# Optimization experiments

Measured on AMD Instinct MI355X. Metric: run time of the kernel, lower is better.

The kernel has to match this reference:

```python
import jax, jax.numpy as jnp
import numpy as np

N_NODES = 50000
N_EDGES = 600000


def gcn_conv(x, src, dst, W, b, num_nodes):
    # x: [N, Cin] -> [N, Cout]; symmetric-normalized GCN with self-loops
    h = x @ W  # [N, Cout]
    loop = jnp.arange(num_nodes, dtype=src.dtype)
    s = jnp.concatenate([src, loop])
    d = jnp.concatenate([dst, loop])
    ones = jnp.ones(s.shape[0], dtype=h.dtype)
    deg = jax.ops.segment_sum(ones, d, num_segments=num_nodes)  # in-degree incl self-loop
    dinv = jnp.where(deg > 0, jax.lax.rsqrt(deg), 0.0)
    norm = dinv[s] * dinv[d]  # [E+N]
    msg = h[s] * norm[:, None]  # gather + scale
    out = jax.ops.segment_sum(msg, d, num_segments=num_nodes)  # scatter-add
    return out + b


def setup_inputs() -> dict:
    key = jax.random.key(0)
    k1, k2, k3, k4 = jax.random.split(key, 4)
    x = jax.random.normal(k1, (N_NODES, 128), dtype=jnp.float32)
    edge_index = jax.random.randint(k2, (2, N_EDGES), 0, N_NODES, dtype=jnp.int64)
    W1 = jax.random.normal(k3, (128, 128), dtype=jnp.float32) * (1.0 / np.sqrt(128))
    b1 = jnp.zeros((128,), dtype=jnp.float32)
    W2 = jax.random.normal(k4, (128, 64), dtype=jnp.float32) * (1.0 / np.sqrt(128))
    b2 = jnp.zeros((64,), dtype=jnp.float32)
    return {"x": x, "edge_index": edge_index, "W1": W1, "b1": b1, "W2": W2, "b2": b2}


def reference(x, edge_index, W1, b1, W2, b2):
    src, dst = edge_index[0], edge_index[1]
    h = gcn_conv(x, src, dst, W1, b1, N_NODES)
    h = jax.nn.relu(h)
    out = gcn_conv(h, src, dst, W2, b2, N_NODES)
    return out
```

## Files before the change

### kernel.cpp

```cpp
#include <hip/hip_runtime.h>
#include <hip/hip_fp16.h>
#include <cstddef>
#include <cstdint>

#define N_NODES 50000
#define N_EDGES 600000
#define M_TILES 3125
#define GEMM_BLKS 782
#define NBUCK 196
#define BUCK_CAP 4096
#define ROUTE_EDGES 2048
#define ROUTE_BLKS 293

typedef short bf16x8 __attribute__((ext_vector_type(8)));
typedef float f32x4 __attribute__((ext_vector_type(4)));


__device__ __forceinline__ unsigned short f32_to_bf16(float x) {
  unsigned u = __float_as_uint(x);
  u += 0x7FFFu + ((u >> 16) & 1u);
  return (unsigned short)(u >> 16);
}
__device__ __forceinline__ float bf16_to_f32(unsigned short h) {
  return __uint_as_float((unsigned)h << 16);
}
__device__ __forceinline__ float bf16_lo(unsigned g) {
  return __uint_as_float(g << 16);
}
__device__ __forceinline__ float bf16_hi(unsigned g) {
  return __uint_as_float(g & 0xFFFF0000u);
}
__device__ __forceinline__ float pk_w(unsigned pk) {
  return __half2float(__ushort_as_half((unsigned short)(pk >> 16)));
}

__device__ __forceinline__ void split8(const float* __restrict__ p, bf16x8& hi,
                                       bf16x8& lo) {
  const float4 v0 = *(const float4*)p;
  const float4 v1 = *(const float4*)(p + 4);
  float v[8] = {v0.x, v0.y, v0.z, v0.w, v1.x, v1.y, v1.z, v1.w};
#pragma unroll
  for (int i = 0; i < 8; i++) {
    const unsigned short h = f32_to_bf16(v[i]);
    hi[i] = (short)h;
    lo[i] = (short)f32_to_bf16(v[i] - bf16_to_f32(h));
  }
}

template <int COUT>
__device__ __forceinline__ void gemm_body(const int wtile, const int lane,
                                          const float* __restrict__ X,
                                          const unsigned short* __restrict__ Wph,
                                          const unsigned short* __restrict__ Wpl,
                                          unsigned short* __restrict__ Hs) {
  constexpr int CT = COUT / 16;
  const int m = lane & 15;
  const int q = lane >> 4;

  f32x4 acc[CT];
#pragma unroll
  for (int ct = 0; ct < CT; ct++) acc[ct] = {0.f, 0.f, 0.f, 0.f};

  const float* xp = X + (size_t)(wtile * 16 + m) * 128 + q * 8;

#pragma unroll
  for (int ks = 0; ks < 4; ks++) {
    bf16x8 ah, al;
    split8(xp + ks * 32, ah, al);
#pragma unroll
    for (int ct = 0; ct < CT; ct++) {
      const size_t bo = ((size_t)(ct * 4 + ks) * 64 + lane) * 8;
      const bf16x8 bh = *(const bf16x8*)(Wph + bo);
      const bf16x8 bl = *(const bf16x8*)(Wpl + bo);
      acc[ct] = __builtin_amdgcn_mfma_f32_16x16x32_bf16(ah, bh, acc[ct], 0, 0, 0);
      acc[ct] = __builtin_amdgcn_mfma_f32_16x16x32_bf16(al, bh, acc[ct], 0, 0, 0);
      acc[ct] = __builtin_amdgcn_mfma_f32_16x16x32_bf16(ah, bl, acc[ct], 0, 0, 0);
    }
  }
#pragma unroll
  for (int ct = 0; ct < CT; ct++) {
#pragma unroll
    for (int r = 0; r < 4; r++) {
      const int orow = wtile * 16 + q * 4 + r;
      Hs[(size_t)orow * COUT + ct * 16 + m] = f32_to_bf16(acc[ct][r]);
    }
  }
}

__device__ __forceinline__ void wpack_body(const int i,
                                           const float* __restrict__ W1,
                                           const float* __restrict__ W2,
                                           unsigned short* __restrict__ w1h,
                                           unsigned short* __restrict__ w1l,
                                           unsigned short* __restrict__ w2h,
                                           unsigned short* __restrict__ w2l) {
  const float* W;
  unsigned short *wh, *wl;
  int o, cout;
  if (i < 16384) {
    W = W1; wh = w1h; wl = w1l; o = i; cout = 128;
  } else {
    W = W2; wh = w2h; wl = w2l; o = i - 16384; cout = 64;
  }
  const int j = o & 7;
  const int ln = (o >> 3) & 63;
  const int t = o >> 9;
  const int ks = t & 3;
  const int ct = t >> 2;
  const int k = ks * 32 + (ln >> 4) * 8 + j;
  const int n = ct * 16 + (ln & 15);
  const float v = W[k * cout + n];
  const unsigned short h = f32_to_bf16(v);
  wh[o] = h;
  wl[o] = f32_to_bf16(v - bf16_to_f32(h));
}

__global__ __launch_bounds__(256) void k_prep_route(
    const float* __restrict__ W1, const float* __restrict__ W2,
    unsigned short* __restrict__ w1h, unsigned short* __restrict__ w1l,
    unsigned short* __restrict__ w2h, unsigned short* __restrict__ w2l,
    const int* __restrict__ src, const int* __restrict__ dst,
    int* __restrict__ cursor, int* __restrict__ counts,
    unsigned* __restrict__ routed) {
  __shared__ int hist[NBUCK];
  __shared__ int lcur[NBUCK];
  const int tid = threadIdx.x;
  if (blockIdx.x < 96) {
    wpack_body(blockIdx.x * 256 + tid, W1, W2, w1h, w1l, w2h, w2l);
  } else {
    const int rb = blockIdx.x - 96;
    for (int t = tid; t < NBUCK; t += 256) hist[t] = 0;
    __syncthreads();
    unsigned packed[8];
    bool cvalid[2];
    const int base = rb * ROUTE_EDGES;
#pragma unroll
    for (int c = 0; c < 2; c++) {
      const int i4 = base + c * 1024 + tid * 4;
      cvalid[c] = (i4 < N_EDGES);
      if (cvalid[c]) {
        const int4 d4 = *(const int4*)(dst + i4);
        const int4 s4 = *(const int4*)(src + i4);
        packed[c * 4 + 0] = ((unsigned)d4.x << 16) | (unsigned)s4.x;
        packed[c * 4 + 1] = ((unsigned)d4.y << 16) | (unsigned)s4.y;
        packed[c * 4 + 2] = ((unsigned)d4.z << 16) | (unsigned)s4.z;
        packed[c * 4 + 3] = ((unsigned)d4.w << 16) | (unsigned)s4.w;
#pragma unroll
        for (int j = 0; j < 4; j++) {
          const unsigned pk = packed[c * 4 + j];
          atomicAdd(&hist[pk >> 24], 1);
          atomicAdd(&counts[pk >> 16], 1);
        }
      }
    }
    __syncthreads();
    for (int t = tid; t < NBUCK; t += 256)
      lcur[t] = t * BUCK_CAP + atomicAdd(&cursor[t], hist[t]);
    __syncthreads();
#pragma unroll
    for (int c = 0; c < 2; c++) {
      if (cvalid[c]) {
#pragma unroll
        for (int j = 0; j < 4; j++) {
          const unsigned pk = packed[c * 4 + j];
          const int slot = atomicAdd(&lcur[pk >> 24], 1);
          routed[slot] = pk;
        }
      }
    }
  }
}

__global__ __launch_bounds__(256) void k_bsort_gemm128(
    const unsigned* __restrict__ routed, const int* __restrict__ cursor,
    const int* __restrict__ counts, int* __restrict__ start,
    int* __restrict__ sorted_src, const float* __restrict__ X,
    const unsigned short* __restrict__ Wph,
    const unsigned short* __restrict__ Wpl, unsigned short* __restrict__ Hs) {
  __shared__ unsigned ebuf[BUCK_CAP];
  __shared__ int h2[256];
  __shared__ int c2[256];
  const int tid = threadIdx.x;
  if (blockIdx.x < NBUCK) {
    const int b = blockIdx.x;
    const int n = cursor[b];
    for (int i = tid; i < n; i += 256) ebuf[i] = routed[b * BUCK_CAP + i];
    h2[tid] = 0;
    __syncthreads();
    for (int i = tid; i < n; i += 256)
      atomicAdd(&h2[(ebuf[i] >> 16) & 255], 1);
    __syncthreads();
    const int own = h2[tid];
    for (int s = 1; s < 256; s <<= 1) {
      const int t = (tid >= s) ? h2[tid - s] : 0;
      __syncthreads();
      h2[tid] += t;
      __syncthreads();
    }
    const int pfx = h2[tid] - own;
    c2[tid] = pfx;
    const int d = b * 256 + tid;
    if (d < N_NODES) start[d] = b * BUCK_CAP + pfx;
    __syncthreads();
    for (int i = tid; i < n; i += 256) {
      const unsigned pk = ebuf[i];
      const int r = atomicAdd(&c2[(pk >> 16) & 255], 1);
      const unsigned si = pk & 0xFFFFu;
      const float rs = rsqrtf((float)counts[si] + 1.0f);
      const unsigned hb = (unsigned)__half_as_ushort(__float2half(rs));
      sorted_src[b * BUCK_CAP + r] = (int)(si | (hb << 16));
    }
  } else {
    const int wtile = (blockIdx.x - NBUCK) * 4 + (tid >> 6);
    if (wtile < M_TILES) gemm_body<128>(wtile, tid & 63, X, Wph, Wpl, Hs);
  }
}

__global__ __launch_bounds__(256) void k_agg128_gemm64(
    const unsigned* __restrict__ Hb, const int* __restrict__ counts,
    const int* __restrict__ start, const int* __restrict__ sorted_src,
    const float* __restrict__ bias, const unsigned short* __restrict__ Wph,
    const unsigned short* __restrict__ Wpl, unsigned short* __restrict__ Hs) {
  __shared__ float a1s[16][132];
  const int lane = threadIdx.x & 63;
  const int wave = threadIdx.x >> 6;
  const int h = lane >> 5;
  const int c = lane & 31;
  const uint2* __restrict__ Hb2 = (const uint2*)Hb;
  const float4 bb = ((const float4*)bias)[c];
  const int vbase = blockIdx.x * 16 + wave * 4;

  const int v0 = vbase + h, v1 = vbase + 2 + h;
  const int deg0 = counts[v0], deg1 = counts[v1];
  const int e00 = start[v0], e01 = start[v1];
  const float dv0 = rsqrtf((float)deg0 + 1.f);
  const float dv1 = rsqrtf((float)deg1 + 1.f);
  const uint2 gs0 = Hb2[(size_t)v0 * 32 + c];
  const uint2 gs1 = Hb2[(size_t)v1 * 32 + c];
  const int pk0 = (c < deg0) ? sorted_src[e00 + c] : 0;
  const int pk1 = (c < deg1) ? sorted_src[e01 + c] : 0;

#pragma unroll
  for (int p = 0; p < 2; p++) {
    const int deg = p ? deg1 : deg0;
    const int e0 = p ? e01 : e00;
    const float dv = p ? dv1 : dv0;
    const uint2 gs = p ? gs1 : gs0;
    const int pk = p ? pk1 : pk0;

    const int dA = __shfl(deg, 0);
    const int dB = __shfl(deg, 32);
    const int mm = max(dA, dB);
    const int m = min(mm, 32);
    const float dv2 = dv * dv;
    float a0 = bf16_lo(gs.x) * dv2;
    float a1 = bf16_hi(gs.x) * dv2;
    float a2 = bf16_lo(gs.y) * dv2;
    float a3 = bf16_hi(gs.y) * dv2;

    for (int j = 0; j < m; j += 8) {
      unsigned pkt[8];
      float w[8];
      uint2 g[8];
#pragma unroll
      for (int t = 0; t < 8; t++)
        pkt[t] = (unsigned)__shfl(pk, (lane & 32) | (j + t));
#pragma unroll
      for (int t = 0; t < 8; t++)
        g[t] = Hb2[(size_t)(pkt[t] & 0xFFFFu) * 32 + c];
#pragma unroll
      for (int t = 0; t < 8; t++) w[t] = pk_w(pkt[t]) * dv;
#pragma unroll
      for (int t = 0; t < 8; t++) {
        a0 += bf16_lo(g[t].x) * w[t];
        a1 += bf16_hi(g[t].x) * w[t];
        a2 += bf16_lo(g[t].y) * w[t];
        a3 += bf16_hi(g[t].y) * w[t];
      }
    }
    for (int base = 32; base < mm; base += 32) {
      int pk2 = 0;
      if (base + c < deg) pk2 = sorted_src[e0 + base + c];
      const int lim = min(32, mm - base);
      for (int k = 0; k < lim; k++) {
        const unsigned pt = (unsigned)__shfl(pk2, (lane & 32) | k);
        const uint2 g = Hb2[(size_t)(pt & 0xFFFFu) * 32 + c];
        const float w = pk_w(pt) * dv;
        a0 += bf16_lo(g.x) * w;
        a1 += bf16_hi(g.x) * w;
        a2 += bf16_lo(g.y) * w;
        a3 += bf16_hi(g.y) * w;
      }
    }
    float4 r;
    r.x = fmaxf(a0 + bb.x, 0.f);
    r.y = fmaxf(a1 + bb.y, 0.f);
    r.z = fmaxf(a2 + bb.z, 0.f);
    r.w = fmaxf(a3 + bb.w, 0.f);
    *(float4*)&a1s[wave * 4 + 2 * p + h][c * 4] = r;
  }
  __syncthreads();

  const int ct = wave;
  const int m2 = lane & 15;
  const int q = lane >> 4;
  f32x4 acc = {0.f, 0.f, 0.f, 0.f};
#pragma unroll
  for (int ks = 0; ks < 4; ks++) {
    bf16x8 ah, al;
    split8(&a1s[m2][ks * 32 + q * 8], ah, al);
    const size_t bo = ((size_t)(ct * 4 + ks) * 64 + lane) * 8;
    const bf16x8 bh = *(const bf16x8*)(Wph + bo);
    const bf16x8 bl = *(const bf16x8*)(Wpl + bo);
    acc = __builtin_amdgcn_mfma_f32_16x16x32_bf16(ah, bh, acc, 0, 0, 0);
    acc = __builtin_amdgcn_mfma_f32_16x16x32_bf16(al, bh, acc, 0, 0, 0);
    acc = __builtin_amdgcn_mfma_f32_16x16x32_bf16(ah, bl, acc, 0, 0, 0);
  }
#pragma unroll
  for (int r = 0; r < 4; r++) {
    const int orow = blockIdx.x * 16 + q * 4 + r;
    Hs[(size_t)orow * 64 + ct * 16 + m2] = f32_to_bf16(acc[r]);
  }
}

__global__ __launch_bounds__(256) void k_agg64(
    const unsigned* __restrict__ Hb, const int* __restrict__ counts,
    const int* __restrict__ start, const int* __restrict__ sorted_src,
    const float* __restrict__ bias, float* __restrict__ out) {
  const int lane = threadIdx.x & 63;
  const int wave = threadIdx.x >> 6;
  const int qq = lane >> 4;
  const int c = lane & 15;
  const uint2* __restrict__ Hb2 = (const uint2*)Hb;
  const float4 bb = ((const float4*)bias)[c];

  const int v = blockIdx.x * 16 + wave * 4 + qq;
  const int deg = counts[v];
  const int e0 = start[v];
  const float dv = rsqrtf((float)deg + 1.0f);
  const uint2 gs = Hb2[(size_t)v * 16 + c];
  const int pk0 = (c < deg) ? sorted_src[e0 + c] : 0;
  const int pk1 = (c + 16 < deg) ? sorted_src[e0 + c + 16] : 0;

  const int d0 = __shfl(deg, 0);
  const int d1 = __shfl(deg, 16);
  const int d2 = __shfl(deg, 32);
  const int d3 = __shfl(deg, 48);
  const int mm = max(max(d0, d1), max(d2, d3));
  const int m = min(mm, 32);
  const float dv2 = dv * dv;
  float a0 = bf16_lo(gs.x) * dv2;
  float a1 = bf16_hi(gs.x) * dv2;
  float a2 = bf16_lo(gs.y) * dv2;
  float a3 = bf16_hi(gs.y) * dv2;

#pragma unroll
  for (int jb = 0; jb < 4; jb++) {
    if (jb * 8 < m) {
      unsigned pkt[8];
      float w[8];
      uint2 g[8];
#pragma unroll
      for (int t = 0; t < 8; t++) {
        const int e = jb * 8 + t;
        const int srcl = (lane & 48) | (e & 15);
        pkt[t] = (unsigned)__shfl((jb < 2) ? pk0 : pk1, srcl);
      }
#pragma unroll
      for (int t = 0; t < 8; t++)
        g[t] = Hb2[(size_t)(pkt[t] & 0xFFFFu) * 16 + c];
#pragma unroll
      for (int t = 0; t < 8; t++) w[t] = pk_w(pkt[t]) * dv;
#pragma unroll
      for (int t = 0; t < 8; t++) {
        a0 += bf16_lo(g[t].x) * w[t];
        a1 += bf16_hi(g[t].x) * w[t];
        a2 += bf16_lo(g[t].y) * w[t];
        a3 += bf16_hi(g[t].y) * w[t];
      }
    }
  }
  for (int base = 32; base < mm; base += 16) {
    int pk2 = 0;
    if (base + c < deg) pk2 = sorted_src[e0 + base + c];
    const int lim = min(16, mm - base);
    for (int k = 0; k < lim; k++) {
      const unsigned pt = (unsigned)__shfl(pk2, (lane & 48) | k);
      const uint2 g = Hb2[(size_t)(pt & 0xFFFFu) * 16 + c];
      const float w = pk_w(pt) * dv;
      a0 += bf16_lo(g.x) * w;
      a1 += bf16_hi(g.x) * w;
      a2 += bf16_lo(g.y) * w;
      a3 += bf16_hi(g.y) * w;
    }
  }
  float4 r;
  r.x = a0 + bb.x;
  r.y = a1 + bb.y;
  r.z = a2 + bb.z;
  r.w = a3 + bb.w;
  ((float4*)out)[(size_t)v * 16 + c] = r;
}


extern "C" void kernel_launch(void* const* d_in, const int* in_sizes, int n_in,
                              void* d_out, int out_size, void* d_ws, size_t ws_size,
                              hipStream_t stream) {
  const float* x = (const float*)d_in[0];
  const int* ei = (const int*)d_in[1];
  const float* W1 = (const float*)d_in[2];
  const float* b1 = (const float*)d_in[3];
  const float* W2 = (const float*)d_in[4];
  const float* b2 = (const float*)d_in[5];
  const int* src = ei;
  const int* dst = ei + N_EDGES;

  char* p = (char*)d_ws;
  auto alloc = [&](size_t bytes) {
    char* q = p;
    p += (bytes + 255) & ~(size_t)255;
    return q;
  };
  int* cursor = (int*)alloc((size_t)NBUCK * 4);
  int* counts = (int*)alloc((size_t)N_NODES * 4);
  unsigned* routed = (unsigned*)alloc((size_t)NBUCK * BUCK_CAP * 4);
  int* sorted_src = (int*)alloc((size_t)NBUCK * BUCK_CAP * 4);
  int* start = (int*)alloc((size_t)N_NODES * 4);
  unsigned short* w1h = (unsigned short*)alloc(16384 * 2);
  unsigned short* w1l = (unsigned short*)alloc(16384 * 2);
  unsigned short* w2h = (unsigned short*)alloc(8192 * 2);
  unsigned short* w2l = (unsigned short*)alloc(8192 * 2);
  unsigned short* h1b = (unsigned short*)alloc((size_t)N_NODES * 128 * 2);
  unsigned short* h2b = (unsigned short*)alloc((size_t)N_NODES * 64 * 2);

  const size_t zlen = (size_t)((char*)counts - (char*)cursor) + (size_t)N_NODES * 4;
  hipMemsetAsync(cursor, 0, zlen, stream);
  hipLaunchKernelGGL(k_prep_route, dim3(96 + ROUTE_BLKS), dim3(256), 0, stream,
                     W1, W2, w1h, w1l, w2h, w2l, src, dst, cursor, counts,
                     routed);
  hipLaunchKernelGGL(k_bsort_gemm128, dim3(NBUCK + GEMM_BLKS), dim3(256), 0,
                     stream, routed, cursor, counts, start, sorted_src, x, w1h,
                     w1l, h1b);
  hipLaunchKernelGGL(k_agg128_gemm64, dim3(M_TILES), dim3(256), 0, stream,
                     (const unsigned*)h1b, counts, start, sorted_src, b1, w2h,
                     w2l, h2b);
  hipLaunchKernelGGL(k_agg64, dim3(M_TILES), dim3(256), 0, stream,
                     (const unsigned*)h2b, counts, start, sorted_src, b2,
                     (float*)d_out);
}
```

Before: 170.0 us.

## Derive degree counts from bucket histogram and defer source-norm packing to aggregation

```diff
diff --git a/kernel.cpp b/kernel.cpp
--- a/kernel.cpp
+++ b/kernel.cpp
@@ -32,6 +32,9 @@
 }
 __device__ __forceinline__ float pk_w(unsigned pk) {
   return __half2float(__ushort_as_half((unsigned short)(pk >> 16)));
+}
+__device__ __forceinline__ int pack_si(int si, float dinv) {
+  return si | ((int)__half_as_ushort(__float2half(dinv)) << 16);
 }
 
 __device__ __forceinline__ void split8(const float* __restrict__ p, bf16x8& hi,
@@ -120,8 +123,7 @@
     unsigned short* __restrict__ w1h, unsigned short* __restrict__ w1l,
     unsigned short* __restrict__ w2h, unsigned short* __restrict__ w2l,
     const int* __restrict__ src, const int* __restrict__ dst,
-    int* __restrict__ cursor, int* __restrict__ counts,
-    unsigned* __restrict__ routed) {
+    int* __restrict__ cursor, unsigned* __restrict__ routed) {
   __shared__ int hist[NBUCK];
   __shared__ int lcur[NBUCK];
   const int tid = threadIdx.x;
@@ -146,11 +148,8 @@
         packed[c * 4 + 2] = ((unsigned)d4.z << 16) | (unsigned)s4.z;
         packed[c * 4 + 3] = ((unsigned)d4.w << 16) | (unsigned)s4.w;
 #pragma unroll
-        for (int j = 0; j < 4; j++) {
-          const unsigned pk = packed[c * 4 + j];
-          atomicAdd(&hist[pk >> 24], 1);
-          atomicAdd(&counts[pk >> 16], 1);
-        }
+        for (int j = 0; j < 4; j++)
+          atomicAdd(&hist[packed[c * 4 + j] >> 24], 1);
       }
     }
     __syncthreads();
@@ -173,7 +172,7 @@
 
 __global__ __launch_bounds__(256) void k_bsort_gemm128(
     const unsigned* __restrict__ routed, const int* __restrict__ cursor,
-    const int* __restrict__ counts, int* __restrict__ start,
+    int* __restrict__ counts, int* __restrict__ start,
     int* __restrict__ sorted_src, const float* __restrict__ X,
     const unsigned short* __restrict__ Wph,
     const unsigned short* __restrict__ Wpl, unsigned short* __restrict__ Hs) {
@@ -200,15 +199,15 @@
     const int pfx = h2[tid] - own;
     c2[tid] = pfx;
     const int d = b * 256 + tid;
-    if (d < N_NODES) start[d] = b * BUCK_CAP + pfx;
+    if (d < N_NODES) {
+      counts[d] = own;
+      start[d] = b * BUCK_CAP + pfx;
+    }
     __syncthreads();
     for (int i = tid; i < n; i += 256) {
       const unsigned pk = ebuf[i];
       const int r = atomicAdd(&c2[(pk >> 16) & 255], 1);
-      const unsigned si = pk & 0xFFFFu;
-      const float rs = rsqrtf((float)counts[si] + 1.0f);
-      const unsigned hb = (unsigned)__half_as_ushort(__float2half(rs));
-      sorted_src[b * BUCK_CAP + r] = (int)(si | (hb << 16));
+      sorted_src[b * BUCK_CAP + r] = (int)(pk & 0xFFFFu);
     }
   } else {
     const int wtile = (blockIdx.x - NBUCK) * 4 + (tid >> 6);
@@ -218,7 +217,7 @@
 
 __global__ __launch_bounds__(256) void k_agg128_gemm64(
     const unsigned* __restrict__ Hb, const int* __restrict__ counts,
-    const int* __restrict__ start, const int* __restrict__ sorted_src,
+    const int* __restrict__ start, int* __restrict__ sorted_src,
     const float* __restrict__ bias, const unsigned short* __restrict__ Wph,
     const unsigned short* __restrict__ Wpl, unsigned short* __restrict__ Hs) {
   __shared__ float a1s[16][132];
@@ -237,8 +236,18 @@
   const float dv1 = rsqrtf((float)deg1 + 1.f);
   const uint2 gs0 = Hb2[(size_t)v0 * 32 + c];
   const uint2 gs1 = Hb2[(size_t)v1 * 32 + c];
-  const int pk0 = (c < deg0) ? sorted_src[e00 + c] : 0;
-  const int pk1 = (c < deg1) ? sorted_src[e01 + c] : 0;
+  int si0 = 0, si1 = 0;
+  float di0 = 0.f, di1 = 0.f;
+  if (c < deg0) {
+    si0 = sorted_src[e00 + c];
+    di0 = rsqrtf((float)counts[si0] + 1.f);
+  }
+  if (c < deg1) {
+    si1 = sorted_src[e01 + c];
+    di1 = rsqrtf((float)counts[si1] + 1.f);
+  }
+  if (c < deg0) sorted_src[e00 + c] = pack_si(si0, di0);
+  if (c < deg1) sorted_src[e01 + c] = pack_si(si1, di1);
 
 #pragma unroll
   for (int p = 0; p < 2; p++) {
@@ -246,7 +255,8 @@
     const int e0 = p ? e01 : e00;
     const float dv = p ? dv1 : dv0;
     const uint2 gs = p ? gs1 : gs0;
-    const int pk = p ? pk1 : pk0;
+    const int si = p ? si1 : si0;
+    const float wi = (p ? di1 : di0) * dv;
 
     const int dA = __shfl(deg, 0);
     const int dB = __shfl(deg, 32);
@@ -259,17 +269,16 @@
     float a3 = bf16_hi(gs.y) * dv2;
 
     for (int j = 0; j < m; j += 8) {
-      unsigned pkt[8];
+      int s[8];
       float w[8];
       uint2 g[8];
 #pragma unroll
-      for (int t = 0; t < 8; t++)
-        pkt[t] = (unsigned)__shfl(pk, (lane & 32) | (j + t));
-#pragma unroll
-      for (int t = 0; t < 8; t++)
-        g[t] = Hb2[(size_t)(pkt[t] & 0xFFFFu) * 32 + c];
-#pragma unroll
-      for (int t = 0; t < 8; t++) w[t] = pk_w(pkt[t]) * dv;
+      for (int t = 0; t < 8; t++) {
+        s[t] = __shfl(si, (lane & 32) | (j + t));
+        w[t] = __shfl(wi, (lane & 32) | (j + t));
+      }
+#pragma unroll
+      for (int t = 0; t < 8; t++) g[t] = Hb2[(size_t)s[t] * 32 + c];
 #pragma unroll
       for (int t = 0; t < 8; t++) {
         a0 += bf16_lo(g[t].x) * w[t];
@@ -279,13 +288,19 @@
       }
     }
     for (int base = 32; base < mm; base += 32) {
-      int pk2 = 0;
-      if (base + c < deg) pk2 = sorted_src[e0 + base + c];
+      int sit = 0;
+      float dit = 0.f;
+      if (base + c < deg) {
+        sit = sorted_src[e0 + base + c];
+        dit = rsqrtf((float)counts[sit] + 1.0f);
+        sorted_src[e0 + base + c] = pack_si(sit, dit);
+      }
+      const float wit = dit * dv;
       const int lim = min(32, mm - base);
       for (int k = 0; k < lim; k++) {
-        const unsigned pt = (unsigned)__shfl(pk2, (lane & 32) | k);
-        const uint2 g = Hb2[(size_t)(pt & 0xFFFFu) * 32 + c];
-        const float w = pk_w(pt) * dv;
+        const int s = __shfl(sit, (lane & 32) | k);
+        const float w = __shfl(wit, (lane & 32) | k);
+        const uint2 g = Hb2[(size_t)s * 32 + c];
         a0 += bf16_lo(g.x) * w;
         a1 += bf16_hi(g.x) * w;
         a2 += bf16_lo(g.y) * w;
@@ -422,9 +437,9 @@
     return q;
   };
   int* cursor = (int*)alloc((size_t)NBUCK * 4);
-  int* counts = (int*)alloc((size_t)N_NODES * 4);
   unsigned* routed = (unsigned*)alloc((size_t)NBUCK * BUCK_CAP * 4);
   int* sorted_src = (int*)alloc((size_t)NBUCK * BUCK_CAP * 4);
+  int* counts = (int*)alloc((size_t)N_NODES * 4);
   int* start = (int*)alloc((size_t)N_NODES * 4);
   unsigned short* w1h = (unsigned short*)alloc(16384 * 2);
   unsigned short* w1l = (unsigned short*)alloc(16384 * 2);
@@ -433,11 +448,9 @@
   unsigned short* h1b = (unsigned short*)alloc((size_t)N_NODES * 128 * 2);
   unsigned short* h2b = (unsigned short*)alloc((size_t)N_NODES * 64 * 2);
 
-  const size_t zlen = (size_t)((char*)counts - (char*)cursor) + (size_t)N_NODES * 4;
-  hipMemsetAsync(cursor, 0, zlen, stream);
+  hipMemsetAsync(cursor, 0, (size_t)NBUCK * 4, stream);
   hipLaunchKernelGGL(k_prep_route, dim3(96 + ROUTE_BLKS), dim3(256), 0, stream,
-                     W1, W2, w1h, w1l, w2h, w2l, src, dst, cursor, counts,
-                     routed);
+                     W1, W2, w1h, w1l, w2h, w2l, src, dst, cursor, routed);
   hipLaunchKernelGGL(k_bsort_gemm128, dim3(NBUCK + GEMM_BLKS), dim3(256), 0,
                      stream, routed, cursor, counts, start, sorted_src, x, w1h,
                      w1l, h1b);
```

Result: faster. 146.9 us (-13.6%).

## Derive degrees from bucket histogram and defer dinv packing to first aggregation

Applied to the files above, without the earlier changes.

```diff
diff --git a/kernel.cpp b/kernel.cpp
--- a/kernel.cpp
+++ b/kernel.cpp
@@ -120,8 +120,7 @@
     unsigned short* __restrict__ w1h, unsigned short* __restrict__ w1l,
     unsigned short* __restrict__ w2h, unsigned short* __restrict__ w2l,
     const int* __restrict__ src, const int* __restrict__ dst,
-    int* __restrict__ cursor, int* __restrict__ counts,
-    unsigned* __restrict__ routed) {
+    int* __restrict__ cursor, unsigned* __restrict__ routed) {
   __shared__ int hist[NBUCK];
   __shared__ int lcur[NBUCK];
   const int tid = threadIdx.x;
@@ -146,11 +145,8 @@
         packed[c * 4 + 2] = ((unsigned)d4.z << 16) | (unsigned)s4.z;
         packed[c * 4 + 3] = ((unsigned)d4.w << 16) | (unsigned)s4.w;
 #pragma unroll
-        for (int j = 0; j < 4; j++) {
-          const unsigned pk = packed[c * 4 + j];
-          atomicAdd(&hist[pk >> 24], 1);
-          atomicAdd(&counts[pk >> 16], 1);
-        }
+        for (int j = 0; j < 4; j++)
+          atomicAdd(&hist[packed[c * 4 + j] >> 24], 1);
       }
     }
     __syncthreads();
@@ -173,7 +169,7 @@
 
 __global__ __launch_bounds__(256) void k_bsort_gemm128(
     const unsigned* __restrict__ routed, const int* __restrict__ cursor,
-    const int* __restrict__ counts, int* __restrict__ start,
+    int2* __restrict__ meta, unsigned short* __restrict__ dinvh,
     int* __restrict__ sorted_src, const float* __restrict__ X,
     const unsigned short* __restrict__ Wph,
     const unsigned short* __restrict__ Wpl, unsigned short* __restrict__ Hs) {
@@ -200,15 +196,15 @@
     const int pfx = h2[tid] - own;
     c2[tid] = pfx;
     const int d = b * 256 + tid;
-    if (d < N_NODES) start[d] = b * BUCK_CAP + pfx;
+    if (d < N_NODES) {
+      meta[d] = make_int2(own, b * BUCK_CAP + pfx);
+      dinvh[d] = __half_as_ushort(__float2half(rsqrtf((float)own + 1.0f)));
+    }
     __syncthreads();
     for (int i = tid; i < n; i += 256) {
       const unsigned pk = ebuf[i];
       const int r = atomicAdd(&c2[(pk >> 16) & 255], 1);
-      const unsigned si = pk & 0xFFFFu;
-      const float rs = rsqrtf((float)counts[si] + 1.0f);
-      const unsigned hb = (unsigned)__half_as_ushort(__float2half(rs));
-      sorted_src[b * BUCK_CAP + r] = (int)(si | (hb << 16));
+      sorted_src[b * BUCK_CAP + r] = (int)(pk & 0xFFFFu);
     }
   } else {
     const int wtile = (blockIdx.x - NBUCK) * 4 + (tid >> 6);
@@ -217,8 +213,8 @@
 }
 
 __global__ __launch_bounds__(256) void k_agg128_gemm64(
-    const unsigned* __restrict__ Hb, const int* __restrict__ counts,
-    const int* __restrict__ start, const int* __restrict__ sorted_src,
+    const unsigned* __restrict__ Hb, const int2* __restrict__ meta,
+    const unsigned short* __restrict__ dinvh, int* __restrict__ sorted_src,
     const float* __restrict__ bias, const unsigned short* __restrict__ Wph,
     const unsigned short* __restrict__ Wpl, unsigned short* __restrict__ Hs) {
   __shared__ float a1s[16][132];
@@ -231,14 +227,24 @@
   const int vbase = blockIdx.x * 16 + wave * 4;
 
   const int v0 = vbase + h, v1 = vbase + 2 + h;
-  const int deg0 = counts[v0], deg1 = counts[v1];
-  const int e00 = start[v0], e01 = start[v1];
+  const int2 md0 = meta[v0], md1 = meta[v1];
+  const int deg0 = md0.x, deg1 = md1.x;
+  const int e00 = md0.y, e01 = md1.y;
   const float dv0 = rsqrtf((float)deg0 + 1.f);
   const float dv1 = rsqrtf((float)deg1 + 1.f);
   const uint2 gs0 = Hb2[(size_t)v0 * 32 + c];
   const uint2 gs1 = Hb2[(size_t)v1 * 32 + c];
-  const int pk0 = (c < deg0) ? sorted_src[e00 + c] : 0;
-  const int pk1 = (c < deg1) ? sorted_src[e01 + c] : 0;
+  int pk0 = 0, pk1 = 0;
+  if (c < deg0) {
+    const int si = sorted_src[e00 + c];
+    pk0 = si | ((int)dinvh[si] << 16);
+    sorted_src[e00 + c] = pk0;
+  }
+  if (c < deg1) {
+    const int si = sorted_src[e01 + c];
+    pk1 = si | ((int)dinvh[si] << 16);
+    sorted_src[e01 + c] = pk1;
+  }
 
 #pragma unroll
   for (int p = 0; p < 2; p++) {
@@ -279,11 +285,15 @@
       }
     }
     for (int base = 32; base < mm; base += 32) {
-      int pk2 = 0;
-      if (base + c < deg) pk2 = sorted_src[e0 + base + c];
+      int pkt2 = 0;
+      if (base + c < deg) {
+        const int sit = sorted_src[e0 + base + c];
+        pkt2 = sit | ((int)dinvh[sit] << 16);
+        sorted_src[e0 + base + c] = pkt2;
+      }
       const int lim = min(32, mm - base);
       for (int k = 0; k < lim; k++) {
-        const unsigned pt = (unsigned)__shfl(pk2, (lane & 32) | k);
+        const unsigned pt = (unsigned)__shfl(pkt2, (lane & 32) | k);
         const uint2 g = Hb2[(size_t)(pt & 0xFFFFu) * 32 + c];
         const float w = pk_w(pt) * dv;
         a0 += bf16_lo(g.x) * w;
@@ -324,8 +334,8 @@
 }
 
 __global__ __launch_bounds__(256) void k_agg64(
-    const unsigned* __restrict__ Hb, const int* __restrict__ counts,
-    const int* __restrict__ start, const int* __restrict__ sorted_src,
+    const unsigned* __restrict__ Hb, const int2* __restrict__ meta,
+    const int* __restrict__ start_unused, const int* __restrict__ sorted_src,
     const float* __restrict__ bias, float* __restrict__ out) {
   const int lane = threadIdx.x & 63;
   const int wave = threadIdx.x >> 6;
@@ -335,8 +345,9 @@
   const float4 bb = ((const float4*)bias)[c];
 
   const int v = blockIdx.x * 16 + wave * 4 + qq;
-  const int deg = counts[v];
-  const int e0 = start[v];
+  const int2 md = meta[v];
+  const int deg = md.x;
+  const int e0 = md.y;
   const float dv = rsqrtf((float)deg + 1.0f);
   const uint2 gs = Hb2[(size_t)v * 16 + c];
   const int pk0 = (c < deg) ? sorted_src[e0 + c] : 0;
@@ -422,10 +433,10 @@
     return q;
   };
   int* cursor = (int*)alloc((size_t)NBUCK * 4);
-  int* counts = (int*)alloc((size_t)N_NODES * 4);
   unsigned* routed = (unsigned*)alloc((size_t)NBUCK * BUCK_CAP * 4);
   int* sorted_src = (int*)alloc((size_t)NBUCK * BUCK_CAP * 4);
-  int* start = (int*)alloc((size_t)N_NODES * 4);
+  int2* meta = (int2*)alloc((size_t)N_NODES * 8);
+  unsigned short* dinvh = (unsigned short*)alloc((size_t)N_NODES * 2);
   unsigned short* w1h = (unsigned short*)alloc(16384 * 2);
   unsigned short* w1l = (unsigned short*)alloc(16384 * 2);
   unsigned short* w2h = (unsigned short*)alloc(8192 * 2);
@@ -433,18 +444,16 @@
   unsigned short* h1b = (unsigned short*)alloc((size_t)N_NODES * 128 * 2);
   unsigned short* h2b = (unsigned short*)alloc((size_t)N_NODES * 64 * 2);
 
-  const size_t zlen = (size_t)((char*)counts - (char*)cursor) + (size_t)N_NODES * 4;
-  hipMemsetAsync(cursor, 0, zlen, stream);
+  hipMemsetAsync(cursor, 0, (size_t)NBUCK * 4, stream);
   hipLaunchKernelGGL(k_prep_route, dim3(96 + ROUTE_BLKS), dim3(256), 0, stream,
-                     W1, W2, w1h, w1l, w2h, w2l, src, dst, cursor, counts,
-                     routed);
+                     W1, W2, w1h, w1l, w2h, w2l, src, dst, cursor, routed);
   hipLaunchKernelGGL(k_bsort_gemm128, dim3(NBUCK + GEMM_BLKS), dim3(256), 0,
-                     stream, routed, cursor, counts, start, sorted_src, x, w1h,
+                     stream, routed, cursor, meta, dinvh, sorted_src, x, w1h,
                      w1l, h1b);
   hipLaunchKernelGGL(k_agg128_gemm64, dim3(M_TILES), dim3(256), 0, stream,
-                     (const unsigned*)h1b, counts, start, sorted_src, b1, w2h,
+                     (const unsigned*)h1b, meta, dinvh, sorted_src, b1, w2h,
                      w2l, h2b);
   hipLaunchKernelGGL(k_agg64, dim3(M_TILES), dim3(256), 0, stream,
-                     (const unsigned*)h2b, counts, start, sorted_src, b2,
-                     (float*)d_out);
-}
+                     (const unsigned*)h2b, meta, (const int*)nullptr,
+                     sorted_src, b2, (float*)d_out);
+}
```

Result: faster. 147.1 us (-13.4%).
